# Performance work log

Hardware: AMD Instinct MI355X
Metric: run time of the kernel (lower is better)

Reference implementation:

```python
import jax, jax.numpy as jnp
import numpy as np

N_NODES = 50000
N_EDGES = 800000
H = 128   # hidden_dim
E = 64    # edge_dim
LN_EPS = 1e-5


def _layer_norm(x, g, b):
    m = jnp.mean(x, axis=-1, keepdims=True)
    v = jnp.mean(jnp.square(x - m), axis=-1, keepdims=True)
    return (x - m) * jax.lax.rsqrt(v + LN_EPS) * g + b


def _gelu(x):
    return jax.nn.gelu(x, approximate=False)  # torch default exact GELU


def setup_inputs() -> dict:
    key = jax.random.key(0)
    ks = jax.random.split(key, 24)

    def lin(k, fin, fout):
        kw, kb = jax.random.split(k)
        s = 1.0 / np.sqrt(fin)
        W = jax.random.uniform(kw, (fin, fout), jnp.float32, -s, s)
        b = jax.random.uniform(kb, (fout,), jnp.float32, -s, s)
        return W, b

    inp = {}
    inp["x"] = jax.random.normal(ks[0], (N_NODES, H), jnp.float32)
    inp["edge_emb"] = jax.random.normal(ks[1], (N_EDGES, E), jnp.float32)
    inp["time_weight"] = jax.random.uniform(ks[2], (N_EDGES, 1), jnp.float32)
    inp["message_node_scale"] = jax.random.uniform(ks[3], (N_NODES, 1), jnp.float32)
    inp["ln1_g"] = jnp.ones((H,), jnp.float32)
    inp["ln1_b"] = jnp.zeros((H,), jnp.float32)
    inp["ln2_g"] = jnp.ones((H,), jnp.float32)
    inp["ln2_b"] = jnp.zeros((H,), jnp.float32)
    inp["selfW"], inp["selfb"] = lin(ks[4], H, H)
    inp["msgW1"], inp["msgb1"] = lin(ks[5], H + E, H)
    inp["msgW2"], inp["msgb2"] = lin(ks[6], H, H)
    inp["gateW1"], inp["gateb1"] = lin(ks[7], 2 * H + E, H)
    inp["gateW2"], inp["gateb2"] = lin(ks[8], H, 1)
    inp["aggW"], inp["aggb"] = lin(ks[9], H, H)
    inp["ffnW1"], inp["ffnb1"] = lin(ks[10], H, 2 * H)
    inp["ffnW2"], inp["ffnb2"] = lin(ks[11], 2 * H, H)
    inp["edge_src"] = jax.random.randint(ks[12], (N_EDGES,), 0, N_NODES, jnp.int32)
    inp["edge_dst"] = jax.random.randint(ks[13], (N_EDGES,), 0, N_NODES, jnp.int32)
    return inp


def reference(x, edge_emb, time_weight, message_node_scale,
              ln1_g, ln1_b, ln2_g, ln2_b,
              selfW, selfb, msgW1, msgb1, msgW2, msgb2,
              gateW1, gateb1, gateW2, gateb2,
              aggW, aggb, ffnW1, ffnb1, ffnW2, ffnb2,
              edge_src, edge_dst):
    n_nodes = x.shape[0]
    n_edges = edge_dst.shape[0]

    h = _layer_norm(x, ln1_g, ln1_b)
    hs = h[edge_src]  # [NE, H]
    hd = h[edge_dst]  # [NE, H]

    msg = _gelu(jnp.concatenate([hs, edge_emb], -1) @ msgW1 + msgb1) @ msgW2 + msgb2
    gate = jax.nn.sigmoid(
        _gelu(jnp.concatenate([hd, hs, edge_emb], -1) @ gateW1 + gateb1) @ gateW2 + gateb2)
    edge_repr = gate * msg
    edge_repr = edge_repr * time_weight
    edge_scale = 0.5 * (message_node_scale[edge_src] + message_node_scale[edge_dst])
    edge_repr = edge_repr * edge_scale

    agg = jax.ops.segment_sum(edge_repr, edge_dst, num_segments=n_nodes)
    deg = jax.ops.segment_sum(jnp.ones((n_edges, 1), x.dtype), edge_dst,
                              num_segments=n_nodes)
    agg = agg / jnp.maximum(deg, 1.0)

    update = (h @ selfW + selfb) + (agg @ aggW + aggb)
    out = x + update  # residual; dropout is identity at inference

    h2 = _layer_norm(out, ln2_g, ln2_b)
    ffn_update = _gelu(h2 @ ffnW1 + ffnb1) @ ffnW2 + ffnb2
    out = out + ffn_update
    return (out, edge_repr)
```

## Files before the change

### kernel.cpp

```cpp
#include <hip/hip_runtime.h>


typedef __attribute__((ext_vector_type(8))) short short8;
typedef __attribute__((ext_vector_type(4))) float f32x4;

#define NN 50000
#define NEDGE 800000

#define MFMA(a, b, c) __builtin_amdgcn_mfma_f32_16x16x32_bf16(a, b, c, 0, 0, 0)

__device__ __forceinline__ unsigned short f2bf(float f) {
  unsigned int u = __float_as_uint(f);
  u += 0x7fffu + ((u >> 16) & 1u);
  return (unsigned short)(u >> 16);
}
__device__ __forceinline__ float bf2f(unsigned short u) {
  return __uint_as_float((unsigned int)u << 16);
}
__device__ __forceinline__ unsigned int cvtpk(float a, float b) {
  unsigned int d;
  asm("v_cvt_pk_bf16_f32 %0, %1, %2" : "=v"(d) : "v"(a), "v"(b));
  return d;
}
__device__ __forceinline__ unsigned short f2bf1(float a) {
  return (unsigned short)cvtpk(a, a);
}
__device__ __forceinline__ float geluf(float x) {
  const float t = x * fmaf(-0.1029437f, x * x, -2.3022211f);
  return x * __builtin_amdgcn_rcpf(1.0f + exp2f(t));
}
__device__ __forceinline__ short8 ld8(const unsigned short* p) {
  return *reinterpret_cast<const short8*>(p);
}
__device__ __forceinline__ int swz256(int row, int byteoff) {
  return row * 256 + (byteoff ^ ((row & 15) << 4));
}
__device__ __forceinline__ int swz128(int row, int byteoff) {
  return row * 128 + (byteoff ^ ((row & 7) << 4));
}

__device__ __forceinline__ void ln_frags(const float* __restrict__ rowp,
                                         const float* __restrict__ g,
                                         const float* __restrict__ b, int koff,
                                         short8 a[4]) {
  f32x4 v[8];
#pragma unroll
  for (int s = 0; s < 4; s++) {
    v[2 * s] = *reinterpret_cast<const f32x4*>(rowp + s * 32 + koff);
    v[2 * s + 1] = *reinterpret_cast<const f32x4*>(rowp + s * 32 + koff + 4);
  }
  float sm = 0.f;
#pragma unroll
  for (int i = 0; i < 8; i++) sm += v[i][0] + v[i][1] + v[i][2] + v[i][3];
  sm += __shfl_xor(sm, 16);
  sm += __shfl_xor(sm, 32);
  const float mean = sm * 0.0078125f;
  float sq = 0.f;
#pragma unroll
  for (int i = 0; i < 8; i++) {
#pragma unroll
    for (int t = 0; t < 4; t++) {
      const float d = v[i][t] - mean;
      sq += d * d;
    }
  }
  sq += __shfl_xor(sq, 16);
  sq += __shfl_xor(sq, 32);
  const float rs = rsqrtf(sq * 0.0078125f + 1e-5f);
#pragma unroll
  for (int s = 0; s < 4; s++) {
    const f32x4 glo = *reinterpret_cast<const f32x4*>(g + s * 32 + koff);
    const f32x4 ghi = *reinterpret_cast<const f32x4*>(g + s * 32 + koff + 4);
    const f32x4 blo = *reinterpret_cast<const f32x4*>(b + s * 32 + koff);
    const f32x4 bhi = *reinterpret_cast<const f32x4*>(b + s * 32 + koff + 4);
    float y[8];
#pragma unroll
    for (int t = 0; t < 4; t++) {
      y[t] = (v[2 * s][t] - mean) * rs * glo[t] + blo[t];
      y[4 + t] = (v[2 * s + 1][t] - mean) * rs * ghi[t] + bhi[t];
    }
    union { unsigned int u[4]; short8 s8; } pk;
    pk.u[0] = cvtpk(y[0], y[1]);
    pk.u[1] = cvtpk(y[2], y[3]);
    pk.u[2] = cvtpk(y[4], y[5]);
    pk.u[3] = cvtpk(y[6], y[7]);
    a[s] = pk.s8;
  }
}

__global__ __launch_bounds__(256) void prep_kernel(
    const float* __restrict__ selfW, const float* __restrict__ msgW1,
    const float* __restrict__ msgW2, const float* __restrict__ gateW1,
    const float* __restrict__ aggW, const float* __restrict__ ffnW1,
    const float* __restrict__ ffnW2, unsigned short* __restrict__ wts,
    int* __restrict__ cnt) {
  const int idx = blockIdx.x * 256 + threadIdx.x;
  if (idx <= NN) cnt[idx] = 0;
  if (idx < 16384) {
    int n = idx >> 7, k = idx & 127;
    wts[idx] = f2bf(selfW[k * 128 + n]);
  } else if (idx < 32768) {
    int l = idx - 16384, n = l >> 7, k = l & 127;
    wts[idx] = f2bf(aggW[k * 128 + n]);
  } else if (idx < 57344) {
    int l = idx - 32768, n = l / 192, k = l - n * 192;
    wts[idx] = f2bf(msgW1[k * 128 + n]);
  } else if (idx < 73728) {
    int l = idx - 57344, n = l >> 7, k = l & 127;
    wts[idx] = f2bf(msgW2[k * 128 + n]);
  } else if (idx < 114688) {
    int l = idx - 73728, n = l / 320, k = l - n * 320;
    wts[idx] = f2bf(gateW1[k * 128 + n]);
  } else if (idx < 147456) {
    int l = idx - 114688, n = l >> 7, k = l & 127;
    wts[idx] = f2bf(ffnW1[k * 256 + n]);
  } else if (idx < 180224) {
    int l = idx - 147456, n = l >> 8, k = l & 255;
    wts[idx] = f2bf(ffnW2[k * 128 + n]);
  }
}

__global__ __launch_bounds__(256) void node_pre_kernel(
    const float* __restrict__ x, const float* __restrict__ ln1g,
    const float* __restrict__ ln1b, const unsigned short* __restrict__ wts,
    const int* __restrict__ edst, unsigned short* __restrict__ pd,
    unsigned short* __restrict__ psm, float* __restrict__ aggf,
    int* __restrict__ cnt) {
  const int wid = threadIdx.x >> 6, lane = threadIdx.x & 63;
  const int q = lane >> 4, r16 = lane & 15, koff = q * 8;
  const int r0 = blockIdx.x * 64 + wid * 16;
  const int row = min(r0 + r16, NN - 1);
  {
    const int t = blockIdx.x * 256 + threadIdx.x;
    const f32x4 z = (f32x4){0.f, 0.f, 0.f, 0.f};
#pragma unroll
    for (int k = 0; k < 8; k++) {
      const int pos = t + k * 200192;
      if (pos < NN * 32) reinterpret_cast<f32x4*>(aggf)[pos] = z;
    }
#pragma unroll
    for (int k = 0; k < 4; k++) {
      const int e = t + k * 200192;
      if (e < NEDGE) atomicAdd(&cnt[edst[e]], 1);
    }
  }
  const unsigned short* gateW1T = wts + 73728;
  const unsigned short* msgW1T = wts + 32768;
  short8 a[4];
  ln_frags(x + (size_t)row * 128, ln1g, ln1b, koff, a);
  f32x4 acc[3][8];
#pragma unroll
  for (int t = 0; t < 3; t++)
#pragma unroll
    for (int nt = 0; nt < 8; nt++) acc[t][nt] = (f32x4){0.f, 0.f, 0.f, 0.f};
#pragma unroll
  for (int s = 0; s < 4; s++) {
    const int k0 = s * 32 + koff;
#pragma unroll
    for (int nt = 0; nt < 8; nt++) {
      const int c = nt * 16 + r16;
      acc[0][nt] = MFMA(a[s], ld8(gateW1T + c * 320 + k0), acc[0][nt]);
      acc[1][nt] = MFMA(a[s], ld8(gateW1T + c * 320 + 128 + k0), acc[1][nt]);
      acc[2][nt] = MFMA(a[s], ld8(msgW1T + c * 192 + k0), acc[2][nt]);
    }
  }
#pragma unroll
  for (int j = 0; j < 4; j++) {
    const int gr = r0 + q * 4 + j;
    if (gr < NN) {
#pragma unroll
      for (int nt = 0; nt < 8; nt++) {
        const int c = nt * 16 + r16;
        pd[(size_t)gr * 128 + c] = f2bf(acc[0][nt][j]);
        psm[(size_t)gr * 256 + c] = f2bf(acc[1][nt][j]);
        psm[(size_t)gr * 256 + 128 + c] = f2bf(acc[2][nt][j]);
      }
    }
  }
}

__global__ __launch_bounds__(256) void scan_sums_kernel(
    const int* __restrict__ cnt, int* __restrict__ bsum) {
  const int gi = blockIdx.x * 256 + threadIdx.x;
  int v = (gi < NN) ? cnt[gi] : 0;
#pragma unroll
  for (int m = 1; m < 64; m <<= 1) v += __shfl_xor(v, m);
  __shared__ int wsum[4];
  if ((threadIdx.x & 63) == 0) wsum[threadIdx.x >> 6] = v;
  __syncthreads();
  if (threadIdx.x == 0)
    bsum[blockIdx.x] = wsum[0] + wsum[1] + wsum[2] + wsum[3];
}

__global__ __launch_bounds__(256) void scan_final_kernel(
    const int* __restrict__ cnt, const int* __restrict__ bsum,
    int* __restrict__ row_start, int* __restrict__ cursor) {
  const int tid = threadIdx.x, lane = tid & 63, wid = tid >> 6;
  const int gi = blockIdx.x * 256 + tid;
  __shared__ int boff_s;
  __shared__ int wsum[4];
  if (wid == 0) {
    int pre = 0;
    for (int i = lane; i < blockIdx.x; i += 64) pre += bsum[i];
#pragma unroll
    for (int m = 32; m >= 1; m >>= 1) pre += __shfl_xor(pre, m);
    if (lane == 0) boff_s = pre;
  }
  const int val = (gi < NN) ? cnt[gi] : 0;
  int v = val;
#pragma unroll
  for (int d = 1; d < 64; d <<= 1) {
    const int t = __shfl_up(v, d);
    if (lane >= d) v += t;
  }
  if (lane == 63) wsum[wid] = v;
  __syncthreads();
  int woff = 0;
  for (int w = 0; w < wid; ++w) woff += wsum[w];
  const int excl = (v - val) + woff + boff_s;
  if (gi < NN) {
    row_start[gi] = excl;
    cursor[gi] = excl;
  }
  if (gi == NN - 1) row_start[NN] = excl + val;
}

__global__ __launch_bounds__(256) void scatter_kernel(
    const int* __restrict__ esrc, const int* __restrict__ edst,
    const float* __restrict__ tw, const float* __restrict__ mns,
    int* __restrict__ cursor, int4* __restrict__ etab) {
  const int e = blockIdx.x * 256 + threadIdx.x;
  const int si = esrc[e];
  const int di = edst[e];
  const int pos = atomicAdd(&cursor[di], 1);
  const float sc = tw[e] * 0.5f * (mns[si] + mns[di]);
  int4 v;
  v.x = e;
  v.y = si;
  v.z = di;
  v.w = __float_as_int(sc);
  etab[pos] = v;
}

__global__ __launch_bounds__(512, 6) void edge_kernel(
    const float* __restrict__ emb, const int4* __restrict__ etab,
    const unsigned short* __restrict__ pd,
    const unsigned short* __restrict__ psm,
    const unsigned short* __restrict__ wts, const float* __restrict__ msgb1,
    const float* __restrict__ msgb2, const float* __restrict__ gateb1,
    const float* __restrict__ gateW2, const float* __restrict__ gateb2v,
    float* __restrict__ erout, float* __restrict__ aggf) {
  __shared__ __align__(16) char buf[64 * 256 + 64 * 256 + 64 * 128];
  __shared__ float p_s[4][64];
  __shared__ float G_s[64];
  __shared__ float sc_s[64];
  __shared__ int di_s[64], eidx_s[64];

  char* pgp = buf;
  char* pmp = buf + 16384;
  char* embp = buf + 32768;
  float* xbuf = (float*)buf;

  const int tid = threadIdx.x;
  const int lane = tid & 63;
  const int wid = tid >> 6;
  const int q = lane >> 4;
  const int r16 = lane & 15;
  const int koff = q * 8;
  const int mg = wid >> 2;
  const int ng = wid & 3;
  const int e0 = blockIdx.x * 64;

  const unsigned short* gateW1T = wts + 73728;
  const unsigned short* msgW1T = wts + 32768;
  const unsigned short* msgW2T = wts + 57344;

  if (tid < 64) {
    const int4 et = etab[e0 + tid];
    eidx_s[tid] = et.x;
    di_s[tid] = et.z;
    sc_s[tid] = __int_as_float(et.w);
  }

#pragma unroll
  for (int r = 0; r < 2; r++) {
    const int unit = tid + 512 * r;
    const int row = unit >> 4;
    const int c = unit & 15;
    const int4 et = etab[e0 + row];
    const int si = et.y, di = et.z;
    const short8 vd = ld8(pd + (size_t)di * 128 + c * 8);
    const short8 vs = ld8(psm + (size_t)si * 256 + c * 8);
    union { unsigned int u[4]; short8 s; } pk;
#pragma unroll
    for (int h = 0; h < 4; h++) {
      const float f0 =
          bf2f((unsigned short)vd[2 * h]) + bf2f((unsigned short)vs[2 * h]);
      const float f1 = bf2f((unsigned short)vd[2 * h + 1]) +
                       bf2f((unsigned short)vs[2 * h + 1]);
      pk.u[h] = cvtpk(f0, f1);
    }
    *reinterpret_cast<short8*>(pgp + swz256(row, c * 16)) = pk.s;
    *reinterpret_cast<short8*>(pmp + swz256(row, c * 16)) =
        ld8(psm + (size_t)si * 256 + 128 + c * 8);
  }
#pragma unroll
  for (int r = 0; r < 2; r++) {
    const int unit = tid + 512 * r;
    const int row = unit >> 4;
    const int c4 = unit & 15;
    const int e = etab[e0 + row].x;
    const f32x4 v =
        *reinterpret_cast<const f32x4*>(emb + (size_t)e * 64 + c4 * 4);
    uint2 w;
    w.x = cvtpk(v[0], v[1]);
    w.y = cvtpk(v[2], v[3]);
    *reinterpret_cast<uint2*>(embp + swz128(row, c4 * 8)) = w;
  }
  __syncthreads();

  int cc[2];
  float g1[2], w2[2], b1m[2], b2m[2];
#pragma unroll
  for (int i = 0; i < 2; i++) {
    cc[i] = ng * 32 + i * 16 + r16;
    g1[i] = gateb1[cc[i]];
    w2[i] = gateW2[cc[i]];
    b1m[i] = msgb1[cc[i]];
    b2m[i] = msgb2[cc[i]];
  }

  short8 bI[2];
#pragma unroll
  for (int h = 0; h < 8; h++) {
    const int kk = koff + h;
    bI[0][h] = (kk == r16) ? (short)0x3F80 : (short)0;
    bI[1][h] = (kk == r16 + 16) ? (short)0x3F80 : (short)0;
  }

  f32x4 accg[2][2], acc1[2][2];
#pragma unroll
  for (int m = 0; m < 2; m++)
#pragma unroll
    for (int i = 0; i < 2; i++) {
      accg[m][i] = (f32x4){0.f, 0.f, 0.f, 0.f};
      acc1[m][i] = (f32x4){0.f, 0.f, 0.f, 0.f};
    }

  {
    const int kw = ng * 32 + koff;
#pragma unroll
    for (int m = 0; m < 2; m++) {
      const int row = mg * 32 + m * 16 + r16;
      const short8 apg =
          *reinterpret_cast<const short8*>(pgp + swz256(row, kw * 2));
      const short8 apm =
          *reinterpret_cast<const short8*>(pmp + swz256(row, kw * 2));
#pragma unroll
      for (int i = 0; i < 2; i++) {
        accg[m][i] = MFMA(apg, bI[i], accg[m][i]);
        acc1[m][i] = MFMA(apm, bI[i], acc1[m][i]);
      }
    }
  }

#pragma unroll
  for (int s = 0; s < 2; s++) {
    const int k0 = s * 32 + koff;
    short8 a[2];
#pragma unroll
    for (int m = 0; m < 2; m++)
      a[m] = *reinterpret_cast<const short8*>(
          embp + swz128(mg * 32 + m * 16 + r16, k0 * 2));
#pragma unroll
    for (int i = 0; i < 2; i++) {
      const short8 bg = ld8(gateW1T + cc[i] * 320 + 256 + k0);
      const short8 bm = ld8(msgW1T + cc[i] * 192 + 128 + k0);
#pragma unroll
      for (int m = 0; m < 2; m++) {
        accg[m][i] = MFMA(a[m], bg, accg[m][i]);
        acc1[m][i] = MFMA(a[m], bm, acc1[m][i]);
      }
    }
  }

#pragma unroll
  for (int m = 0; m < 2; m++) {
#pragma unroll
    for (int j = 0; j < 4; j++) {
      const int row = mg * 32 + m * 16 + q * 4 + j;
      float v = geluf(accg[m][0][j] + g1[0]) * w2[0] +
                geluf(accg[m][1][j] + g1[1]) * w2[1];
      v += __shfl_xor(v, 1);
      v += __shfl_xor(v, 2);
      v += __shfl_xor(v, 4);
      v += __shfl_xor(v, 8);
      if (r16 == 0) p_s[ng][row] = v;
    }
  }

#pragma unroll
  for (int m = 0; m < 2; m++) {
#pragma unroll
    for (int i = 0; i < 2; i++) {
#pragma unroll
      for (int j = 0; j < 4; j++) {
        const int row = mg * 32 + m * 16 + q * 4 + j;
        *reinterpret_cast<unsigned short*>(pmp + swz256(row, cc[i] * 2)) =
            f2bf1(geluf(acc1[m][i][j] + b1m[i]));
      }
    }
  }
  __syncthreads();

  if (tid < 64) {
    const float p = gateb2v[0] + p_s[0][tid] + p_s[1][tid] + p_s[2][tid] +
                    p_s[3][tid];
    G_s[tid] =
        sc_s[tid] * __builtin_amdgcn_rcpf(1.f + exp2f(-1.4426950f * p));
  }

  f32x4 acc2[2][2];
#pragma unroll
  for (int m = 0; m < 2; m++)
#pragma unroll
    for (int i = 0; i < 2; i++) acc2[m][i] = (f32x4){0.f, 0.f, 0.f, 0.f};
#pragma unroll
  for (int s = 0; s < 4; s++) {
    const int k0 = s * 32 + koff;
    short8 a[2];
#pragma unroll
    for (int m = 0; m < 2; m++)
      a[m] = *reinterpret_cast<const short8*>(
          pmp + swz256(mg * 32 + m * 16 + r16, k0 * 2));
#pragma unroll
    for (int i = 0; i < 2; i++) {
      const short8 b = ld8(msgW2T + cc[i] * 128 + k0);
#pragma unroll
      for (int m = 0; m < 2; m++) acc2[m][i] = MFMA(a[m], b, acc2[m][i]);
    }
  }
  __syncthreads();

#pragma unroll
  for (int m = 0; m < 2; m++)
#pragma unroll
    for (int i = 0; i < 2; i++)
#pragma unroll
      for (int j = 0; j < 4; j++) {
        const int row = mg * 32 + m * 16 + q * 4 + j;
        xbuf[row * 132 + cc[i]] = G_s[row] * (acc2[m][i][j] + b2m[i]);
      }
  __syncthreads();

#pragma unroll
  for (int u = 0; u < 4; u++) {
    const int unit = tid + u * 512;
    const int r = unit >> 5;
    const int f4 = unit & 31;
    const f32x4 val = *reinterpret_cast<const f32x4*>(&xbuf[r * 132 + f4 * 4]);
    *reinterpret_cast<f32x4*>(erout + (size_t)eidx_s[r] * 128 + f4 * 4) = val;
  }

  {
    const int col = tid & 127;
    const int qt = tid >> 7;
    const int rbeg = qt * 16, rend = rbeg + 16;
    float acc = 0.f;
    int prev = di_s[rbeg];
    for (int r = rbeg; r < rend; ++r) {
      const int d = di_s[r];
      if (d != prev) {
        atomicAdd(&aggf[(size_t)prev * 128 + col], acc);
        acc = 0.f;
        prev = d;
      }
      acc += xbuf[r * 132 + col];
    }
    atomicAdd(&aggf[(size_t)prev * 128 + col], acc);
  }
}

__global__ __launch_bounds__(256) void node_ffn_kernel(
    const float* __restrict__ x, const float* __restrict__ ln1g,
    const float* __restrict__ ln1b, const float* __restrict__ aggf,
    const int* __restrict__ row_start, const unsigned short* __restrict__ wts,
    const float* __restrict__ selfb, const float* __restrict__ aggb,
    const float* __restrict__ ln2g, const float* __restrict__ ln2b,
    const float* __restrict__ fb1, const float* __restrict__ fb2,
    float* __restrict__ outp) {
  __shared__ unsigned short h2s[4][16 * 136];
  __shared__ unsigned short ts[4][16 * 264];
  const int wid = threadIdx.x >> 6, lane = threadIdx.x & 63;
  const int q = lane >> 4, r16 = lane & 15, koff = q * 8;
  const int r0 = blockIdx.x * 64 + wid * 16;
  const int row = min(r0 + r16, NN - 1);
  const float inv = __builtin_amdgcn_rcpf(
      fmaxf((float)(row_start[row + 1] - row_start[row]), 1.0f));
  const unsigned short* selfWT = wts;
  const unsigned short* aggWT = wts + 16384;
  const unsigned short* W1T = wts + 114688;
  const unsigned short* W2T = wts + 147456;

  short8 a1[4];
  ln_frags(x + (size_t)row * 128, ln1g, ln1b, koff, a1);
  f32x4 acc[8];
#pragma unroll
  for (int nt = 0; nt < 8; nt++) acc[nt] = (f32x4){0.f, 0.f, 0.f, 0.f};
#pragma unroll
  for (int s = 0; s < 4; s++) {
    const int k0 = s * 32 + koff;
    const float* ap = aggf + (size_t)row * 128 + k0;
    const f32x4 f0 = *reinterpret_cast<const f32x4*>(ap);
    const f32x4 f1 = *reinterpret_cast<const f32x4*>(ap + 4);
    union { unsigned int u[4]; short8 s; } pk;
    pk.u[0] = cvtpk(f0[0] * inv, f0[1] * inv);
    pk.u[1] = cvtpk(f0[2] * inv, f0[3] * inv);
    pk.u[2] = cvtpk(f1[0] * inv, f1[1] * inv);
    pk.u[3] = cvtpk(f1[2] * inv, f1[3] * inv);
#pragma unroll
    for (int nt = 0; nt < 8; nt++) {
      acc[nt] = MFMA(a1[s], ld8(selfWT + (nt * 16 + r16) * 128 + k0), acc[nt]);
      acc[nt] = MFMA(pk.s, ld8(aggWT + (nt * 16 + r16) * 128 + k0), acc[nt]);
    }
  }

  float o[8][4];
#pragma unroll
  for (int j = 0; j < 4; j++) {
    const int gr = min(r0 + q * 4 + j, NN - 1);
#pragma unroll
    for (int nt = 0; nt < 8; nt++) {
      const int c = r16 + 16 * nt;
      o[nt][j] = x[(size_t)gr * 128 + c] + acc[nt][j] + selfb[c] + aggb[c];
    }
  }

#pragma unroll
  for (int j = 0; j < 4; j++) {
    float s1 = 0.f;
#pragma unroll
    for (int nt = 0; nt < 8; nt++) s1 += o[nt][j];
    s1 += __shfl_xor(s1, 1);
    s1 += __shfl_xor(s1, 2);
    s1 += __shfl_xor(s1, 4);
    s1 += __shfl_xor(s1, 8);
    const float mean = s1 * 0.0078125f;
    float s2 = 0.f;
#pragma unroll
    for (int nt = 0; nt < 8; nt++) {
      const float d = o[nt][j] - mean;
      s2 += d * d;
    }
    s2 += __shfl_xor(s2, 1);
    s2 += __shfl_xor(s2, 2);
    s2 += __shfl_xor(s2, 4);
    s2 += __shfl_xor(s2, 8);
    const float rs = rsqrtf(s2 * 0.0078125f + 1e-5f);
#pragma unroll
    for (int nt = 0; nt < 8; nt++) {
      const int c = r16 + 16 * nt;
      h2s[wid][(q * 4 + j) * 136 + c] =
          f2bf1((o[nt][j] - mean) * rs * ln2g[c] + ln2b[c]);
    }
  }

  f32x4 acc1[16];
#pragma unroll
  for (int nt = 0; nt < 16; nt++) acc1[nt] = (f32x4){0.f, 0.f, 0.f, 0.f};
#pragma unroll
  for (int s = 0; s < 4; s++) {
    const int k0 = s * 32 + koff;
    const short8 a =
        *reinterpret_cast<const short8*>(&h2s[wid][r16 * 136 + k0]);
#pragma unroll
    for (int nt = 0; nt < 16; nt++)
      acc1[nt] = MFMA(a, ld8(W1T + (nt * 16 + r16) * 128 + k0), acc1[nt]);
  }
#pragma unroll
  for (int nt = 0; nt < 16; nt++) {
    const int c = r16 + 16 * nt;
    const float bb = fb1[c];
#pragma unroll
    for (int j = 0; j < 4; j++)
      ts[wid][(q * 4 + j) * 264 + c] = f2bf1(geluf(acc1[nt][j] + bb));
  }

  f32x4 acc2[8];
#pragma unroll
  for (int nt = 0; nt < 8; nt++) acc2[nt] = (f32x4){0.f, 0.f, 0.f, 0.f};
#pragma unroll
  for (int s = 0; s < 8; s++) {
    const int k0 = s * 32 + koff;
    const short8 av =
        *reinterpret_cast<const short8*>(&ts[wid][r16 * 264 + k0]);
#pragma unroll
    for (int nt = 0; nt < 8; nt++)
      acc2[nt] = MFMA(av, ld8(W2T + (nt * 16 + r16) * 256 + k0), acc2[nt]);
  }

#pragma unroll
  for (int j = 0; j < 4; j++) {
    const int gr = r0 + q * 4 + j;
    if (gr < NN) {
#pragma unroll
      for (int nt = 0; nt < 8; nt++) {
        const int c = r16 + 16 * nt;
        outp[(size_t)gr * 128 + c] = o[nt][j] + acc2[nt][j] + fb2[c];
      }
    }
  }
}

extern "C" void kernel_launch(void* const* d_in, const int* in_sizes, int n_in,
                              void* d_out, int out_size, void* d_ws,
                              size_t ws_size, hipStream_t stream) {
  (void)in_sizes; (void)n_in; (void)out_size; (void)ws_size;
  const float* x = (const float*)d_in[0];
  const float* emb = (const float*)d_in[1];
  const float* tw = (const float*)d_in[2];
  const float* mns = (const float*)d_in[3];
  const float* ln1g = (const float*)d_in[4];
  const float* ln1b = (const float*)d_in[5];
  const float* ln2g = (const float*)d_in[6];
  const float* ln2b = (const float*)d_in[7];
  const float* selfW = (const float*)d_in[8];
  const float* selfb = (const float*)d_in[9];
  const float* msgW1 = (const float*)d_in[10];
  const float* msgb1 = (const float*)d_in[11];
  const float* msgW2 = (const float*)d_in[12];
  const float* msgb2 = (const float*)d_in[13];
  const float* gateW1 = (const float*)d_in[14];
  const float* gateb1 = (const float*)d_in[15];
  const float* gateW2 = (const float*)d_in[16];
  const float* gateb2 = (const float*)d_in[17];
  const float* aggW = (const float*)d_in[18];
  const float* aggb = (const float*)d_in[19];
  const float* ffnW1 = (const float*)d_in[20];
  const float* ffnb1 = (const float*)d_in[21];
  const float* ffnW2 = (const float*)d_in[22];
  const float* ffnb2 = (const float*)d_in[23];
  const int* esrc = (const int*)d_in[24];
  const int* edst = (const int*)d_in[25];

  char* ws = (char*)d_ws;
  unsigned short* pdb = (unsigned short*)(ws);
  unsigned short* psmb = (unsigned short*)(ws + 25600000);
  unsigned short* wts = (unsigned short*)(ws + 76800000);
  int* cnt = (int*)(ws + 77160448);
  int* row_start = (int*)(ws + 77360640);
  int* cursor = (int*)(ws + 77560832);
  int* bsum = (int*)(ws + 77761024);
  int4* etab = (int4*)(ws + 77763072);

  float* out_nodes = (float*)d_out;
  float* out_edges = out_nodes + (size_t)NN * 128;
  float* aggf = out_nodes;

  const int NB_SCAN = (NN + 255) / 256;

  prep_kernel<<<704, 256, 0, stream>>>(selfW, msgW1, msgW2, gateW1, aggW,
                                       ffnW1, ffnW2, wts, cnt);
  node_pre_kernel<<<782, 256, 0, stream>>>(x, ln1g, ln1b, wts, edst, pdb,
                                           psmb, aggf, cnt);
  scan_sums_kernel<<<NB_SCAN, 256, 0, stream>>>(cnt, bsum);
  scan_final_kernel<<<NB_SCAN, 256, 0, stream>>>(cnt, bsum, row_start, cursor);
  scatter_kernel<<<3125, 256, 0, stream>>>(esrc, edst, tw, mns, cursor, etab);
  edge_kernel<<<12500, 512, 0, stream>>>(emb, etab, pdb, psmb, wts, msgb1,
                                         msgb2, gateb1, gateW2, gateb2,
                                         out_edges, aggf);
  node_ffn_kernel<<<782, 256, 0, stream>>>(x, ln1g, ln1b, aggf, row_start,
                                           wts, selfb, aggb, ln2g, ln2b,
                                           ffnb1, ffnb2, out_nodes);
}
```

Before: 582.5 us.

## Shrink edge kernel LDS footprint and raise occupancy target to 8 blocks

Drops the separate shared arrays for edge indices, scale, gate partials and G, and aliases the gate partials and G into dead regions of the main staging buffer. The per-edge fields are now reloaded from the edge table in global memory instead of being cached in LDS. The launch bound goes from 6 to 8 blocks per CU so more waves can be resident. In exchange there are extra global/L2 loads of the edge table, an added barrier to guard the aliased region, and tighter register limits that could cause spills.

```diff
diff --git a/kernel.cpp b/kernel.cpp
--- a/kernel.cpp
+++ b/kernel.cpp
@@ -242,7 +242,7 @@
   etab[pos] = v;
 }
 
-__global__ __launch_bounds__(512, 6) void edge_kernel(
+__global__ __launch_bounds__(512, 8) void edge_kernel(
     const float* __restrict__ emb, const int4* __restrict__ etab,
     const unsigned short* __restrict__ pd,
     const unsigned short* __restrict__ psm,
@@ -250,15 +250,13 @@
     const float* __restrict__ msgb2, const float* __restrict__ gateb1,
     const float* __restrict__ gateW2, const float* __restrict__ gateb2v,
     float* __restrict__ erout, float* __restrict__ aggf) {
-  __shared__ __align__(16) char buf[64 * 256 + 64 * 256 + 64 * 128];
-  __shared__ float p_s[4][64];
-  __shared__ float G_s[64];
-  __shared__ float sc_s[64];
-  __shared__ int di_s[64], eidx_s[64];
+  __shared__ __align__(16) char buf[40960];
 
   char* pgp = buf;
   char* pmp = buf + 16384;
   char* embp = buf + 32768;
+  float* p_s = (float*)(buf + 4096);
+  float* G = (float*)(buf + 33792);
   float* xbuf = (float*)buf;
 
   const int tid = threadIdx.x;
@@ -274,13 +272,6 @@
   const unsigned short* gateW1T = wts + 73728;
   const unsigned short* msgW1T = wts + 32768;
   const unsigned short* msgW2T = wts + 57344;
-
-  if (tid < 64) {
-    const int4 et = etab[e0 + tid];
-    eidx_s[tid] = et.x;
-    di_s[tid] = et.z;
-    sc_s[tid] = __int_as_float(et.w);
-  }
 
 #pragma unroll
   for (int r = 0; r < 2; r++) {
@@ -383,6 +374,7 @@
       }
     }
   }
+  __syncthreads();
 
 #pragma unroll
   for (int m = 0; m < 2; m++) {
@@ -395,7 +387,7 @@
       v += __shfl_xor(v, 2);
       v += __shfl_xor(v, 4);
       v += __shfl_xor(v, 8);
-      if (r16 == 0) p_s[ng][row] = v;
+      if (r16 == 0) p_s[ng * 64 + row] = v;
     }
   }
 
@@ -414,10 +406,10 @@
   __syncthreads();
 
   if (tid < 64) {
-    const float p = gateb2v[0] + p_s[0][tid] + p_s[1][tid] + p_s[2][tid] +
-                    p_s[3][tid];
-    G_s[tid] =
-        sc_s[tid] * __builtin_amdgcn_rcpf(1.f + exp2f(-1.4426950f * p));
+    const float sc = __int_as_float(etab[e0 + tid].w);
+    const float p = gateb2v[0] + p_s[tid] + p_s[64 + tid] + p_s[128 + tid] +
+                    p_s[192 + tid];
+    G[tid] = sc * __builtin_amdgcn_rcpf(1.f + exp2f(-1.4426950f * p));
   }
 
   f32x4 acc2[2][2];
@@ -449,7 +441,7 @@
 #pragma unroll
       for (int j = 0; j < 4; j++) {
         const int row = mg * 32 + m * 16 + q * 4 + j;
-        xbuf[row * 132 + cc[i]] = G_s[row] * (acc2[m][i][j] + b2m[i]);
+        xbuf[row * 132 + cc[i]] = G[row] * (acc2[m][i][j] + b2m[i]);
       }
   __syncthreads();
 
@@ -459,7 +451,8 @@
     const int r = unit >> 5;
     const int f4 = unit & 31;
     const f32x4 val = *reinterpret_cast<const f32x4*>(&xbuf[r * 132 + f4 * 4]);
-    *reinterpret_cast<f32x4*>(erout + (size_t)eidx_s[r] * 128 + f4 * 4) = val;
+    *reinterpret_cast<f32x4*>(erout + (size_t)etab[e0 + r].x * 128 + f4 * 4) =
+        val;
   }
 
   {
@@ -467,9 +460,9 @@
     const int qt = tid >> 7;
     const int rbeg = qt * 16, rend = rbeg + 16;
     float acc = 0.f;
-    int prev = di_s[rbeg];
+    int prev = etab[e0 + rbeg].z;
     for (int r = rbeg; r < rend; ++r) {
-      const int d = di_s[r];
+      const int d = etab[e0 + r].z;
       if (d != prev) {
         atomicAdd(&aggf[(size_t)prev * 128 + col], acc);
         acc = 0.f;
```

Measured after the change: 818.1 us. 1.4x slower.
